# Kernel optimization log

Measured on AMD Instinct MI355X. Metric: run time of the kernel, lower is better.

The kernel has to match this reference:

```python
import jax, jax.numpy as jnp
import numpy as np

LAMB = 0.1
SIZE_AVERAGE = True


def setup_inputs() -> dict:
    key = jax.random.key(0)
    k1, k2 = jax.random.split(key)
    N, D = 8192, 4096
    inp = jax.random.normal(k1, (N, D), dtype=jnp.float32)
    target = jax.random.normal(k2, (N, D), dtype=jnp.float32)
    return {"input": inp, "target": target}


def _drae_loss(inp, target, lamb=LAMB, size_average=SIZE_AVERAGE):
    # Per-sample squared reconstruction error: Err[n] = sum_d (inp - target)^2
    err = (inp - target).reshape(inp.shape[0], -1)
    Err = jnp.sum(err * err, axis=1)                      # [N]
    N = Err.shape[0]
    sErr = jnp.sort(Err)                                  # ascending

    # Prefix sums replace the original O(N^2) Python scan.
    cs = jnp.cumsum(sErr)                                 # [N]
    cs2 = jnp.cumsum(sErr * sErr)                         # [N]
    total, total2 = cs[-1], cs2[-1]
    nf = jnp.asarray(N, sErr.dtype)
    allMean = total / nf
    Sb = total2 - nf * allMean * allMean                  # sum (e - allMean)^2

    # Candidate splits: inlier count k = 1..N-1 (loop index i = k-1).
    k = jnp.arange(1, N, dtype=sErr.dtype)                # [N-1]
    csk, cs2k = cs[:-1], cs2[:-1]
    Sw1 = cs2k - csk * csk / k                            # within-inlier scatter
    Sw2 = (total2 - cs2k) - (total - csk) ** 2 / (nf - k) # within-outlier scatter
    obj = (Sw1 + Sw2) / Sb                                # Fisher-style ratio

    i = jnp.argmin(obj)                                   # first min, like strict '<'
    optObj = obj[i]
    T = (i + 1).astype(sErr.dtype)                        # inlier count
    inlier_sum = cs[i]

    out = inlier_sum / T if size_average else inlier_sum
    return out + lamb * optObj


def reference(input, target):
    return _drae_loss(input, target)
```

## Files before the change

kernel.cpp:

```cpp
#include <hip/hip_runtime.h>

#define NROWS 8192
#define NCOLS 4096
#define LAMB  0.1

typedef unsigned int u32;
typedef unsigned long long u64;

__global__ __launch_bounds__(256, 4) void rowerr_kernel(const float* __restrict__ inp,
                                                        const float* __restrict__ tgt,
                                                        float* __restrict__ err) {
    const int lane = threadIdx.x & 63;
    const int wid  = blockIdx.x * 4 + (threadIdx.x >> 6);

#pragma unroll
    for (int rr = 0; rr < 2; ++rr) {
        const int row = wid * 2 + rr;
        const float4* a = reinterpret_cast<const float4*>(inp + (size_t)row * NCOLS);
        const float4* b = reinterpret_cast<const float4*>(tgt + (size_t)row * NCOLS);

        float acc0 = 0.f, acc1 = 0.f, acc2 = 0.f, acc3 = 0.f;
#pragma unroll
        for (int c = 0; c < 16; ++c) {
            const float4 va = a[lane + c * 64];
            const float4 vb = b[lane + c * 64];
            const float dx = va.x - vb.x;
            const float dy = va.y - vb.y;
            const float dz = va.z - vb.z;
            const float dw = va.w - vb.w;
            acc0 += dx * dx;
            acc1 += dy * dy;
            acc2 += dz * dz;
            acc3 += dw * dw;
        }
        float acc = (acc0 + acc1) + (acc2 + acc3);

#pragma unroll
        for (int off = 32; off > 0; off >>= 1) acc += __shfl_down(acc, off, 64);

        if (lane == 0) err[row] = acc;
    }
}

__device__ __forceinline__ double fastrcp(double x) {
    double r = (double)(1.0f / (float)x);
    r = r * (2.0 - x * r);
    r = r * (2.0 - x * r);
    return r;
}

__global__ __launch_bounds__(1024) void drae_kernel(const float* __restrict__ err,
                                                    float* __restrict__ out) {
    const int N = NROWS;
    __shared__ u32 bufA[NROWS];
    __shared__ u32 bufB[NROWS];
    __shared__ u32 hist[16 * 256];
    __shared__ u32 dtot[256], dbase[256];
    __shared__ u32 saux[4];
    __shared__ double auxX[16], auxT2[16], redH[16], redCs[16];
    __shared__ int    redIdx[16];

    const int tid  = threadIdx.x;
    const int lane = tid & 63, wv = tid >> 6;
    const u64 ltmask = (1ull << lane) - 1ull;

#pragma unroll
    for (int k = 0; k < 8; ++k) {
        const int i = tid + k * 1024;
        bufA[i] = __float_as_uint(err[i]);
    }

    u32* src = bufA;
    u32* dst = bufB;

    for (int pass = 0; pass < 4; ++pass) {
        const int shift = pass * 8;

        __syncthreads();
#pragma unroll
        for (int k = 0; k < 4; ++k) hist[tid + k * 1024] = 0;
        __syncthreads();

        u32 key[8], rnk[8];
#pragma unroll
        for (int r = 0; r < 8; ++r) key[r] = src[wv * 512 + r * 64 + lane];

#pragma unroll
        for (int r = 0; r < 8; ++r) {
            const u32 d = (key[r] >> shift) & 255u;
            u64 match = ~0ull;
#pragma unroll
            for (int b = 0; b < 8; ++b) {
                const u64 bb = __ballot((d >> b) & 1u);
                match &= ((d >> b) & 1u) ? bb : ~bb;
            }
            const int within = __popcll(match & ltmask);
            const int leader = __builtin_ctzll(match);
            const u32 base = hist[wv * 256 + d];
            rnk[r] = base + (u32)within;
            if (lane == leader) hist[wv * 256 + d] = base + (u32)__popcll(match);
        }
        __syncthreads();

        if (tid < 256) {
            u32 s = 0;
#pragma unroll
            for (int w = 0; w < 16; ++w) {
                const u32 t = hist[w * 256 + tid];
                hist[w * 256 + tid] = s;
                s += t;
            }
            dtot[tid] = s;
        }
        __syncthreads();

        u32 val = 0, incl = 0;
        if (tid < 256) {
            val  = dtot[tid];
            incl = val;
#pragma unroll
            for (int off = 1; off < 64; off <<= 1) {
                const u32 t = __shfl_up(incl, off, 64);
                if (lane >= off) incl += t;
            }
            if (lane == 63) saux[wv] = incl;
        }
        __syncthreads();
        if (tid < 256) {
            u32 add = 0;
#pragma unroll
            for (int w = 0; w < 4; ++w) if (w < wv) add += saux[w];
            dbase[tid] = incl - val + add;
        }
        __syncthreads();

#pragma unroll
        for (int r = 0; r < 8; ++r) {
            const u32 d = (key[r] >> shift) & 255u;
            dst[dbase[d] + hist[wv * 256 + d] + rnk[r]] = key[r];
        }

        u32* tmp = src; src = dst; dst = tmp;
    }
    __syncthreads();

    float v[8];
#pragma unroll
    for (int r = 0; r < 8; ++r) v[r] = __uint_as_float(src[(tid << 3) + r]);

    double sx = 0.0, sx2 = 0.0;
#pragma unroll
    for (int r = 0; r < 8; ++r) {
        sx  += (double)v[r];
        sx2 += (double)v[r] * (double)v[r];
    }

    double ix = sx;
#pragma unroll
    for (int off = 1; off < 64; off <<= 1) {
        double t1 = __shfl_up(ix, off, 64);
        if (lane >= off) ix += t1;
    }
    double t2 = sx2;
#pragma unroll
    for (int off = 32; off > 0; off >>= 1) t2 += __shfl_xor(t2, off, 64);

    if (lane == 63) auxX[wv]  = ix;
    if (lane == 0)  auxT2[wv] = t2;
    __syncthreads();

    double wOff1 = 0.0, total1 = 0.0, total2 = 0.0;
#pragma unroll
    for (int w = 0; w < 16; ++w) {
        const double a1 = auxX[w];
        if (w < wv) wOff1 += a1;
        total1 += a1;
        total2 += auxT2[w];
    }
    const double exc1 = wOff1 + (ix - sx);
    const double nf = (double)N;

    double run1 = exc1;
    double bestH = -1e300, bestCs = 0.0;
    int bestIdx = N;
#pragma unroll
    for (int r = 0; r < 8; ++r) {
        const int idx = (tid << 3) + r;
        run1 += (double)v[r];
        if (idx < N - 1) {
            const double kf  = (double)(idx + 1);
            const double rem = total1 - run1;
            const double h   = run1 * run1 * fastrcp(kf) +
                               rem  * rem  * fastrcp(nf - kf);
            if (h > bestH) { bestH = h; bestIdx = idx; bestCs = run1; }
        }
    }

#pragma unroll
    for (int off = 32; off > 0; off >>= 1) {
        const double oH   = __shfl_down(bestH, off, 64);
        const int    oIdx = __shfl_down(bestIdx, off, 64);
        const double oCs  = __shfl_down(bestCs, off, 64);
        if (oH > bestH || (oH == bestH && oIdx < bestIdx)) {
            bestH = oH; bestIdx = oIdx; bestCs = oCs;
        }
    }
    if (lane == 0) { redH[wv] = bestH; redIdx[wv] = bestIdx; redCs[wv] = bestCs; }
    __syncthreads();

    if (tid == 0) {
        double bH = redH[0], bCs = redCs[0];
        int bIdx = redIdx[0];
        for (int w = 1; w < 16; ++w) {
            if (redH[w] > bH || (redH[w] == bH && redIdx[w] < bIdx)) {
                bH = redH[w]; bIdx = redIdx[w]; bCs = redCs[w];
            }
        }
        const double Sb     = total2 - total1 * total1 / nf;
        const double optObj = (total2 - bH) / Sb;
        const double T      = (double)(bIdx + 1);
        out[0] = (float)(bCs / T + LAMB * optObj);
    }
}

extern "C" void kernel_launch(void* const* d_in, const int* in_sizes, int n_in,
                              void* d_out, int out_size, void* d_ws, size_t ws_size,
                              hipStream_t stream) {
    const float* inp = (const float*)d_in[0];
    const float* tgt = (const float*)d_in[1];
    float* errbuf = (float*)d_ws;

    rowerr_kernel<<<NROWS / 8, 256, 0, stream>>>(inp, tgt, errbuf);
    drae_kernel<<<1, 1024, 0, stream>>>(errbuf, (float*)d_out);
}
```

Before: 73.96 us.

## Fuse row-error and sort kernels via last-block counter, adaptive radix passes

Merges the row-error reduction and the single-block sort/scan into one kernel. Each block writes its row errors, bumps a global atomic counter, and the last block to finish runs the radix sort and Fisher split search, which removes the second kernel launch. It also range-reduces the keys by subtracting the minimum bit pattern so three radix passes suffice when the range fits in 24 bits, and shrinks the histogram to 16-bit counters. In exchange the main kernel now runs 1024-thread blocks with a large static shared footprint, which may lower occupancy in the bandwidth-bound phase, and a memset launch is added for the counter.

```diff
diff --git a/kernel.cpp b/kernel.cpp
--- a/kernel.cpp
+++ b/kernel.cpp
@@ -3,23 +3,45 @@
 #define NROWS 8192
 #define NCOLS 4096
 #define LAMB  0.1
+#define NBLK  512
+#define RPB   16
 
 typedef unsigned int u32;
+typedef unsigned short u16;
 typedef unsigned long long u64;
 
-__global__ __launch_bounds__(256, 4) void rowerr_kernel(const float* __restrict__ inp,
-                                                        const float* __restrict__ tgt,
-                                                        float* __restrict__ err) {
-    const int lane = threadIdx.x & 63;
-    const int wid  = blockIdx.x * 4 + (threadIdx.x >> 6);
-
-#pragma unroll
-    for (int rr = 0; rr < 2; ++rr) {
-        const int row = wid * 2 + rr;
+__device__ __forceinline__ double fastrcp(double x) {
+    double r = (double)(1.0f / (float)x);
+    r = r * (2.0 - x * r);
+    r = r * (2.0 - x * r);
+    return r;
+}
+
+__global__ __launch_bounds__(1024) void fused_kernel(const float* __restrict__ inp,
+                                                     const float* __restrict__ tgt,
+                                                     float* err, u32* counter,
+                                                     float* __restrict__ out) {
+    const int N = NROWS;
+    __shared__ u32 bufA[NROWS];
+    __shared__ u32 bufB[NROWS];
+    __shared__ u16 hist[16 * 256];
+    __shared__ u32 dtot[256], dbase[256];
+    __shared__ u32 saux[4];
+    __shared__ u32 sMin[16], sMax[16];
+    __shared__ double auxX[16], auxT2[16], redH[16], redCs[16];
+    __shared__ int    redIdx[16];
+    __shared__ int    amLast;
+
+    const int tid  = threadIdx.x;
+    const int lane = tid & 63, wv = tid >> 6;
+    const u64 ltmask = (1ull << lane) - 1ull;
+
+    {
+        const int row = blockIdx.x * RPB + wv;
         const float4* a = reinterpret_cast<const float4*>(inp + (size_t)row * NCOLS);
         const float4* b = reinterpret_cast<const float4*>(tgt + (size_t)row * NCOLS);
 
-        float acc0 = 0.f, acc1 = 0.f, acc2 = 0.f, acc3 = 0.f;
+        float a0 = 0.f, a1 = 0.f, a2 = 0.f, a3 = 0.f;
 #pragma unroll
         for (int c = 0; c < 16; ++c) {
             const float4 va = a[lane + c * 64];
@@ -28,57 +50,63 @@
             const float dy = va.y - vb.y;
             const float dz = va.z - vb.z;
             const float dw = va.w - vb.w;
-            acc0 += dx * dx;
-            acc1 += dy * dy;
-            acc2 += dz * dz;
-            acc3 += dw * dw;
-        }
-        float acc = (acc0 + acc1) + (acc2 + acc3);
-
+            a0 += dx * dx; a1 += dy * dy; a2 += dz * dz; a3 += dw * dw;
+        }
+        float acc = (a0 + a1) + (a2 + a3);
 #pragma unroll
         for (int off = 32; off > 0; off >>= 1) acc += __shfl_down(acc, off, 64);
 
-        if (lane == 0) err[row] = acc;
-    }
-}
-
-__device__ __forceinline__ double fastrcp(double x) {
-    double r = (double)(1.0f / (float)x);
-    r = r * (2.0 - x * r);
-    r = r * (2.0 - x * r);
-    return r;
-}
-
-__global__ __launch_bounds__(1024) void drae_kernel(const float* __restrict__ err,
-                                                    float* __restrict__ out) {
-    const int N = NROWS;
-    __shared__ u32 bufA[NROWS];
-    __shared__ u32 bufB[NROWS];
-    __shared__ u32 hist[16 * 256];
-    __shared__ u32 dtot[256], dbase[256];
-    __shared__ u32 saux[4];
-    __shared__ double auxX[16], auxT2[16], redH[16], redCs[16];
-    __shared__ int    redIdx[16];
-
-    const int tid  = threadIdx.x;
-    const int lane = tid & 63, wv = tid >> 6;
-    const u64 ltmask = (1ull << lane) - 1ull;
-
+        if (lane == 0)
+            __hip_atomic_store(&err[row], acc, __ATOMIC_RELAXED,
+                               __HIP_MEMORY_SCOPE_AGENT);
+    }
+
+    __syncthreads();
+    if (tid == 0) {
+        const u32 old = __hip_atomic_fetch_add(counter, 1u, __ATOMIC_ACQ_REL,
+                                               __HIP_MEMORY_SCOPE_AGENT);
+        amLast = (old == (u32)(NBLK - 1));
+    }
+    __syncthreads();
+    if (!amLast) return;
+
+    u32 bits[8];
+    u32 mn = 0xFFFFFFFFu, mx = 0u;
 #pragma unroll
     for (int k = 0; k < 8; ++k) {
         const int i = tid + k * 1024;
-        bufA[i] = __float_as_uint(err[i]);
-    }
+        const float v = __hip_atomic_load(&err[i], __ATOMIC_RELAXED,
+                                          __HIP_MEMORY_SCOPE_AGENT);
+        bits[k] = __float_as_uint(v);
+        mn = min(mn, bits[k]);
+        mx = max(mx, bits[k]);
+    }
+#pragma unroll
+    for (int off = 32; off > 0; off >>= 1) {
+        mn = min(mn, (u32)__shfl_xor((int)mn, off, 64));
+        mx = max(mx, (u32)__shfl_xor((int)mx, off, 64));
+    }
+    if (lane == 0) { sMin[wv] = mn; sMax[wv] = mx; }
+    __syncthreads();
+    u32 minb = sMin[0], maxb = sMax[0];
+#pragma unroll
+    for (int w = 1; w < 16; ++w) { minb = min(minb, sMin[w]); maxb = max(maxb, sMax[w]); }
+    const int npass = ((maxb - minb) < (1u << 24)) ? 3 : 4;
+
+#pragma unroll
+    for (int k = 0; k < 8; ++k) bufA[tid + k * 1024] = bits[k] - minb;
 
     u32* src = bufA;
     u32* dst = bufB;
 
-    for (int pass = 0; pass < 4; ++pass) {
+    for (int pass = 0; pass < npass; ++pass) {
         const int shift = pass * 8;
 
         __syncthreads();
-#pragma unroll
-        for (int k = 0; k < 4; ++k) hist[tid + k * 1024] = 0;
+        {
+            u32* h32 = reinterpret_cast<u32*>(hist);
+            h32[tid] = 0; h32[tid + 1024] = 0;
+        }
         __syncthreads();
 
         u32 key[8], rnk[8];
@@ -96,9 +124,9 @@
             }
             const int within = __popcll(match & ltmask);
             const int leader = __builtin_ctzll(match);
-            const u32 base = hist[wv * 256 + d];
+            const u32 base = (u32)hist[wv * 256 + d];
             rnk[r] = base + (u32)within;
-            if (lane == leader) hist[wv * 256 + d] = base + (u32)__popcll(match);
+            if (lane == leader) hist[wv * 256 + d] = (u16)(base + (u32)__popcll(match));
         }
         __syncthreads();
 
@@ -106,8 +134,8 @@
             u32 s = 0;
 #pragma unroll
             for (int w = 0; w < 16; ++w) {
-                const u32 t = hist[w * 256 + tid];
-                hist[w * 256 + tid] = s;
+                const u32 t = (u32)hist[w * 256 + tid];
+                hist[w * 256 + tid] = (u16)s;
                 s += t;
             }
             dtot[tid] = s;
@@ -137,7 +165,7 @@
 #pragma unroll
         for (int r = 0; r < 8; ++r) {
             const u32 d = (key[r] >> shift) & 255u;
-            dst[dbase[d] + hist[wv * 256 + d] + rnk[r]] = key[r];
+            dst[dbase[d] + (u32)hist[wv * 256 + d] + rnk[r]] = key[r];
         }
 
         u32* tmp = src; src = dst; dst = tmp;
@@ -146,7 +174,7 @@
 
     float v[8];
 #pragma unroll
-    for (int r = 0; r < 8; ++r) v[r] = __uint_as_float(src[(tid << 3) + r]);
+    for (int r = 0; r < 8; ++r) v[r] = __uint_as_float(src[(tid << 3) + r] + minb);
 
     double sx = 0.0, sx2 = 0.0;
 #pragma unroll
@@ -229,7 +257,9 @@
     const float* inp = (const float*)d_in[0];
     const float* tgt = (const float*)d_in[1];
     float* errbuf = (float*)d_ws;
-
-    rowerr_kernel<<<NROWS / 8, 256, 0, stream>>>(inp, tgt, errbuf);
-    drae_kernel<<<1, 1024, 0, stream>>>(errbuf, (float*)d_out);
+    u32*   counter = (u32*)((char*)d_ws + NROWS * 4);
+
+    hipMemsetAsync(counter, 0, 4, stream);
+    fused_kernel<<<NBLK, 1024, 0, stream>>>(inp, tgt, errbuf, counter,
+                                            (float*)d_out);
 }
```

New measurement: 86.06 us. 1.16x slower.
